# Kernel tuning notes

Hardware: AMD Instinct MI355X
Metric: run time of the kernel (lower is better)

The kernel has to match this reference:

```python
import jax, jax.numpy as jnp
import numpy as np

N = 50000      # nodes
E = 600000     # edges (before self-loops)
D_IN = 128     # input feature dim
HID = 128      # hidden_channels
HEADS1 = 8
OUT1 = HID // HEADS1  # 16 per head, concat -> 128
NEG_SLOPE = 0.2       # PyG GATConv default leaky_relu slope


def setup_inputs() -> dict:
    key = jax.random.key(0)
    ks = jax.random.split(key, 12)
    glorot = lambda k, shape: jax.random.normal(k, shape, jnp.float32) * np.sqrt(2.0 / (shape[0] + shape[-1]))
    x = jax.random.normal(ks[0], (N, D_IN), jnp.float32)
    edge_index = jax.random.randint(ks[1], (2, E), 0, N, dtype=jnp.int64)
    W1 = glorot(ks[2], (D_IN, HEADS1 * OUT1))
    att_src1 = glorot(ks[3], (HEADS1, OUT1))
    att_dst1 = glorot(ks[4], (HEADS1, OUT1))
    b1 = jnp.zeros((HEADS1 * OUT1,), jnp.float32)
    W2 = glorot(ks[5], (HID, HID))
    att_src2 = glorot(ks[6], (1, HID))
    att_dst2 = glorot(ks[7], (1, HID))
    b2 = jnp.zeros((HID,), jnp.float32)
    return {"x": x, "edge_index": edge_index,
            "W1": W1, "att_src1": att_src1, "att_dst1": att_dst1, "b1": b1,
            "W2": W2, "att_src2": att_src2, "att_dst2": att_dst2, "b2": b2}


def gat_conv(x, edge_index, W, a_src, a_dst, bias, concat):
    """PyG-style GATConv (eval mode: attention dropout disabled)."""
    n = x.shape[0]
    heads, out_ch = a_src.shape
    # add self-loops (PyG default add_self_loops=True)
    loop = jnp.arange(n, dtype=edge_index.dtype)
    src = jnp.concatenate([edge_index[0], loop])  # message source
    dst = jnp.concatenate([edge_index[1], loop])  # aggregation target
    h = (x @ W).reshape(n, heads, out_ch)                    # [n, H, C]
    alpha_src = jnp.sum(h * a_src[None], axis=-1)            # [n, H]
    alpha_dst = jnp.sum(h * a_dst[None], axis=-1)            # [n, H]
    e = alpha_src[src] + alpha_dst[dst]                      # [E+n, H]
    e = jnp.where(e > 0, e, NEG_SLOPE * e)                   # leaky_relu
    # segment softmax over incoming edges of each destination node
    e_max = jax.ops.segment_max(e, dst, num_segments=n)      # [n, H]
    ex = jnp.exp(e - e_max[dst])
    denom = jax.ops.segment_sum(ex, dst, num_segments=n)     # [n, H]
    alpha = ex / denom[dst]                                  # [E+n, H]
    msg = h[src] * alpha[:, :, None]                         # [E+n, H, C]
    out = jax.ops.segment_sum(msg, dst, num_segments=n)      # [n, H, C]
    out = out.reshape(n, heads * out_ch) if concat else out.mean(axis=1)
    return out + bias


def reference(x, edge_index, W1, att_src1, att_dst1, b1, W2, att_src2, att_dst2, b2):
    # eval mode: F.dropout is identity
    h = jax.nn.elu(gat_conv(x, edge_index, W1, att_src1, att_dst1, b1, concat=True))
    out = gat_conv(h, edge_index, W2, att_src2, att_dst2, b2, concat=False)
    return out
```

## Files before the change

### kernel.cpp

```cpp
#include <hip/hip_runtime.h>
#include <hip/hip_bf16.h>

#define NEG_SLOPE 0.2f
#define BCAP 8192

typedef short s16x8 __attribute__((ext_vector_type(8)));
typedef float f32x4 __attribute__((ext_vector_type(4)));

__device__ __forceinline__ unsigned short f2bf(float f) {
    unsigned int u = __float_as_uint(f);
    u += 0x7FFFu + ((u >> 16) & 1u);
    return (unsigned short)(u >> 16);
}


__global__ __launch_bounds__(256) void prep_w_kernel(const float* __restrict__ W1,
                                                     const float* __restrict__ as1,
                                                     const float* __restrict__ ad1,
                                                     unsigned short* __restrict__ Wf1,
                                                     const float* __restrict__ W2,
                                                     const float* __restrict__ as2,
                                                     const float* __restrict__ ad2,
                                                     unsigned short* __restrict__ Wf2,
                                                     int* __restrict__ gcursor,
                                                     int* __restrict__ rowptr, int n, int en) {
    int bid = blockIdx.x;
    int t = threadIdx.x;
    if (bid == 8) {
        gcursor[t] = 0;
        if (t == 0) rowptr[n] = en;
        return;
    }
    int layer = bid >> 2;
    int kt = bid & 3;
    const float* W = layer ? W2 : W1;
    const float* as_v = layer ? as2 : as1;
    const float* ad_v = layer ? ad2 : ad1;
    unsigned short* Wf = layer ? Wf2 : Wf1;
    int H = layer ? 1 : 8;
    for (int task = t; task < 9 * 64; task += 256) {
        int ct = task / 64, l = task & 63;
        int kbase = kt * 32 + (l >> 4) * 8;
        int c = l & 15;
        unsigned short o[8];
        if (ct < 8) {
            int col = ct * 16 + c;
#pragma unroll
            for (int j = 0; j < 8; ++j) o[j] = f2bf(W[(size_t)(kbase + j) * 128 + col]);
        } else {
#pragma unroll
            for (int j = 0; j < 8; ++j) {
                float s = 0.f;
                if (H == 8) {
                    const float* a = (c < 8) ? as_v : ad_v;
                    int hh = c & 7;
                    for (int m = 0; m < 16; ++m)
                        s += W[(size_t)(kbase + j) * 128 + hh * 16 + m] * a[hh * 16 + m];
                } else if (c < 2) {
                    const float* a = (c == 0) ? as_v : ad_v;
                    for (int m = 0; m < 128; ++m)
                        s += W[(size_t)(kbase + j) * 128 + m] * a[m];
                }
                o[j] = f2bf(s);
            }
        }
        *(uint4*)&Wf[(((size_t)kt * 9 + ct) * 64 + l) * 8] = *(uint4*)o;
    }
}


__global__ __launch_bounds__(256) void scatter_kernel(const int* __restrict__ ei, int e, int n,
                                                      int* __restrict__ gcursor,
                                                      unsigned int* __restrict__ gpair) {
    __shared__ int lh[256], lbase[256];
    int t = threadIdx.x;
    lh[t] = 0;
    __syncthreads();
    int base = blockIdx.x * 2048;
    int en = e + n;
    int bk[8], rk[8];
    unsigned int pk[8];
#pragma unroll
    for (int q = 0; q < 8; ++q) {
        int i = base + q * 256 + t;
        bk[q] = -1;
        if (i < en) {
            int src, dst;
            if (i < e) { src = ei[i]; dst = ei[e + i]; }
            else       { src = i - e; dst = i - e; }
            int b = dst >> 8;
            bk[q] = b;
            rk[q] = atomicAdd(&lh[b], 1);
            pk[q] = (unsigned int)src | ((unsigned int)(dst & 255) << 16);
        }
    }
    __syncthreads();
    if (lh[t]) lbase[t] = atomicAdd(&gcursor[t], lh[t]);
    __syncthreads();
#pragma unroll
    for (int q = 0; q < 8; ++q)
        if (bk[q] >= 0) gpair[(size_t)bk[q] * BCAP + lbase[bk[q]] + rk[q]] = pk[q];
}


__global__ __launch_bounds__(256) void bucket_csr_kernel(const unsigned int* __restrict__ gpair,
                                                         const int* __restrict__ gcursor,
                                                         int* __restrict__ rowptr,
                                                         int* __restrict__ colsrc, int n) {
    int b = blockIdx.x, t = threadIdx.x;
    __shared__ int bscan[256], cnt[256], scn[256], cur[256];
    int bc = gcursor[t];
    bscan[t] = bc;
    cnt[t] = 0;
    __syncthreads();
    for (int off = 1; off < 256; off <<= 1) {
        int u = (t >= off) ? bscan[t - off] : 0;
        __syncthreads();
        bscan[t] += u;
        __syncthreads();
    }
    int mybase = bscan[b] - gcursor[b];
    int mycnt = gcursor[b];
    const unsigned int* mypair = gpair + (size_t)b * BCAP;
    for (int i = t; i < mycnt; i += 256)
        atomicAdd(&cnt[mypair[i] >> 16], 1);
    __syncthreads();
    int v = cnt[t];
    scn[t] = v;
    __syncthreads();
    for (int off = 1; off < 256; off <<= 1) {
        int u = (t >= off) ? scn[t - off] : 0;
        __syncthreads();
        scn[t] += u;
        __syncthreads();
    }
    int ex = scn[t] - v;
    cur[t] = ex;
    int node = b * 256 + t;
    if (node < n) rowptr[node] = mybase + ex;
    __syncthreads();
    for (int i = t; i < mycnt; i += 256) {
        unsigned int p = mypair[i];
        int ofs = atomicAdd(&cur[p >> 16], 1);
        colsrc[mybase + ofs] = (int)(p & 0xFFFFu);
    }
}


template <int H, bool INBF16>
__global__ __launch_bounds__(256) void gemm_mfma_kernel(const void* __restrict__ Xv,
                                                        const unsigned short* __restrict__ Wf,
                                                        unsigned short* __restrict__ Ob,
                                                        float* __restrict__ as_out,
                                                        float* __restrict__ ad_out, int n) {
    __shared__ unsigned short lds[8192];
    int tid = threadIdx.x;
    int row0 = blockIdx.x * 64;

#pragma unroll
    for (int q = 0; q < 4; ++q) {
        int task = tid + q * 256;
        int r = task >> 4, kc = task & 15;
        int gr = row0 + r;
        uint4 val = make_uint4(0, 0, 0, 0);
        if (gr < n) {
            if (INBF16) {
                val = *(const uint4*)((const unsigned short*)Xv + (size_t)gr * 128 + kc * 8);
            } else {
                const float4* xp = (const float4*)((const float*)Xv + (size_t)gr * 128 + kc * 8);
                float4 x0 = xp[0], x1 = xp[1];
                unsigned short o[8] = {f2bf(x0.x), f2bf(x0.y), f2bf(x0.z), f2bf(x0.w),
                                       f2bf(x1.x), f2bf(x1.y), f2bf(x1.z), f2bf(x1.w)};
                val = *(uint4*)o;
            }
        }
        int w = r >> 4, kt = kc >> 2, lane = ((kc & 3) << 4) + (r & 15);
        *(uint4*)&lds[(size_t)(((w * 4 + kt) * 64) + lane) * 8] = val;
    }
    __syncthreads();

    int w = tid >> 6, l = tid & 63;
    s16x8 a[4];
#pragma unroll
    for (int kt = 0; kt < 4; ++kt)
        a[kt] = *(s16x8*)&lds[(size_t)((w * 4 + kt) * 64 + l) * 8];

    const s16x8* bp = (const s16x8*)Wf;
    f32x4 acc[9];
#pragma unroll
    for (int ct = 0; ct < 9; ++ct) acc[ct] = (f32x4){0.f, 0.f, 0.f, 0.f};
#pragma unroll
    for (int ct = 0; ct < 9; ++ct) {
#pragma unroll
        for (int kt = 0; kt < 4; ++kt) {
            s16x8 b = bp[(kt * 9 + ct) * 64 + l];
            acc[ct] = __builtin_amdgcn_mfma_f32_16x16x32_bf16(a[kt], b, acc[ct], 0, 0, 0);
        }
    }

    int c = l & 15, rgrp = l >> 4;
    int rowb = row0 + w * 16 + rgrp * 4;
#pragma unroll
    for (int reg = 0; reg < 4; ++reg) {
        int row = rowb + reg;
        if (row < n) {
#pragma unroll
            for (int ct = 0; ct < 8; ++ct)
                Ob[(size_t)row * 128 + ct * 16 + c] = f2bf(acc[ct][reg]);
            float av = acc[8][reg];
            if (H == 8) {
                if (c < 8) as_out[(size_t)row * 8 + c] = av;
                else       ad_out[(size_t)row * 8 + (c - 8)] = av;
            } else {
                if (c == 0)      as_out[row] = av;
                else if (c == 1) ad_out[row] = av;
            }
        }
    }
}


template <int H, int OBF>
__global__ __launch_bounds__(256) void agg_kernel(const int* __restrict__ rowptr,
                                                  const int* __restrict__ colsrc,
                                                  const unsigned short* __restrict__ hb,
                                                  const float* __restrict__ as,
                                                  const float* __restrict__ ad,
                                                  const float* __restrict__ bias,
                                                  void* __restrict__ outv, int n) {
    int tid = threadIdx.x;
    int node = blockIdx.x * 16 + (tid >> 4);
    int cl = tid & 15;
    if (node >= n) return;
    int beg = rowptr[node];
    int end = rowptr[node + 1];
    int head = (H == 8) ? (cl >> 1) : 0;
    float adh = ad[(size_t)node * H + head];

    float acc[8];
#pragma unroll
    for (int c = 0; c < 8; ++c) acc[c] = 0.f;
    float den = 0.f;

    int i = beg;
    for (; i + 4 <= end; i += 4) {
        int s0 = colsrc[i], s1 = colsrc[i + 1], s2 = colsrc[i + 2], s3 = colsrc[i + 3];
        float e0 = as[(size_t)s0 * H + head];
        float e1 = as[(size_t)s1 * H + head];
        float e2 = as[(size_t)s2 * H + head];
        float e3 = as[(size_t)s3 * H + head];
        uint4 a0 = *(const uint4*)(hb + (size_t)s0 * 128 + cl * 8);
        uint4 a1 = *(const uint4*)(hb + (size_t)s1 * 128 + cl * 8);
        uint4 a2 = *(const uint4*)(hb + (size_t)s2 * 128 + cl * 8);
        uint4 a3 = *(const uint4*)(hb + (size_t)s3 * 128 + cl * 8);
        float ev, w0, w1, w2, w3;
        ev = e0 + adh; ev = (ev > 0.f) ? ev : NEG_SLOPE * ev; w0 = __expf(ev);
        ev = e1 + adh; ev = (ev > 0.f) ? ev : NEG_SLOPE * ev; w1 = __expf(ev);
        ev = e2 + adh; ev = (ev > 0.f) ? ev : NEG_SLOPE * ev; w2 = __expf(ev);
        ev = e3 + adh; ev = (ev > 0.f) ? ev : NEG_SLOPE * ev; w3 = __expf(ev);
        den += (w0 + w1) + (w2 + w3);
        unsigned int u0[4] = {a0.x, a0.y, a0.z, a0.w};
        unsigned int u1[4] = {a1.x, a1.y, a1.z, a1.w};
        unsigned int u2[4] = {a2.x, a2.y, a2.z, a2.w};
        unsigned int u3[4] = {a3.x, a3.y, a3.z, a3.w};
#pragma unroll
        for (int k = 0; k < 4; ++k) {
            acc[2 * k]     += w0 * __uint_as_float(u0[k] << 16);
            acc[2 * k + 1] += w0 * __uint_as_float(u0[k] & 0xffff0000u);
            acc[2 * k]     += w1 * __uint_as_float(u1[k] << 16);
            acc[2 * k + 1] += w1 * __uint_as_float(u1[k] & 0xffff0000u);
            acc[2 * k]     += w2 * __uint_as_float(u2[k] << 16);
            acc[2 * k + 1] += w2 * __uint_as_float(u2[k] & 0xffff0000u);
            acc[2 * k]     += w3 * __uint_as_float(u3[k] << 16);
            acc[2 * k + 1] += w3 * __uint_as_float(u3[k] & 0xffff0000u);
        }
    }
    for (; i < end; ++i) {
        int s = colsrc[i];
        float ev = as[(size_t)s * H + head] + adh;
        ev = (ev > 0.f) ? ev : NEG_SLOPE * ev;
        float wgt = __expf(ev);
        den += wgt;
        uint4 a = *(const uint4*)(hb + (size_t)s * 128 + cl * 8);
        unsigned int u[4] = {a.x, a.y, a.z, a.w};
#pragma unroll
        for (int k = 0; k < 4; ++k) {
            acc[2 * k]     += wgt * __uint_as_float(u[k] << 16);
            acc[2 * k + 1] += wgt * __uint_as_float(u[k] & 0xffff0000u);
        }
    }

    float inv = 1.0f / den;
    float r[8];
#pragma unroll
    for (int k = 0; k < 8; ++k) {
        r[k] = acc[k] * inv + bias[cl * 8 + k];
        if (OBF) r[k] = (r[k] > 0.f) ? r[k] : expm1f(r[k]);
    }
    if (OBF) {
        unsigned short o[8];
#pragma unroll
        for (int k = 0; k < 8; ++k) o[k] = f2bf(r[k]);
        *(uint4*)((unsigned short*)outv + (size_t)node * 128 + cl * 8) = *(uint4*)o;
    } else {
        float4* p = (float4*)((float*)outv + (size_t)node * 128 + cl * 8);
        p[0] = make_float4(r[0], r[1], r[2], r[3]);
        p[1] = make_float4(r[4], r[5], r[6], r[7]);
    }
}


extern "C" void kernel_launch(void* const* d_in, const int* in_sizes, int n_in,
                              void* d_out, int out_size, void* d_ws, size_t ws_size,
                              hipStream_t stream) {
    const float* x    = (const float*)d_in[0];
    const int*   ei   = (const int*)d_in[1];
    const float* W1   = (const float*)d_in[2];
    const float* a_s1 = (const float*)d_in[3];
    const float* a_d1 = (const float*)d_in[4];
    const float* b1   = (const float*)d_in[5];
    const float* W2   = (const float*)d_in[6];
    const float* a_s2 = (const float*)d_in[7];
    const float* a_d2 = (const float*)d_in[8];
    const float* b2   = (const float*)d_in[9];

    const int n  = in_sizes[0] / 128;
    const int e  = in_sizes[1] / 2;
    const int en = e + n;
    const int nbuck = (n + 255) >> 8;
    const int echunks = (en + 2047) / 2048;

    char* ws = (char*)d_ws;
    size_t off = 0;
    auto alloc = [&](size_t bytes) -> void* {
        void* p = ws + off;
        off += (bytes + 255) & ~(size_t)255;
        return p;
    };
    unsigned short* hb   = (unsigned short*)alloc((size_t)n * 128 * 2);
    unsigned short* hmid = (unsigned short*)alloc((size_t)n * 128 * 2);
    float* as1    = (float*)alloc((size_t)n * 8 * 4);
    float* ad1    = (float*)alloc((size_t)n * 8 * 4);
    float* as2    = (float*)alloc((size_t)n * 4);
    float* ad2    = (float*)alloc((size_t)n * 4);
    int*   rowptr = (int*)alloc((size_t)(n + 1) * 4);
    int*   colsrc = (int*)alloc((size_t)en * 4);
    unsigned int* gpair = (unsigned int*)alloc((size_t)nbuck * BCAP * 4);
    int*   gcursor= (int*)alloc(256 * 4);
    unsigned short* Wf1 = (unsigned short*)alloc(4 * 9 * 64 * 8 * 2);
    unsigned short* Wf2 = (unsigned short*)alloc(4 * 9 * 64 * 8 * 2);

    prep_w_kernel<<<9, 256, 0, stream>>>(W1, a_s1, a_d1, Wf1, W2, a_s2, a_d2, Wf2,
                                         gcursor, rowptr, n, en);
    scatter_kernel<<<echunks, 256, 0, stream>>>(ei, e, n, gcursor, gpair);
    bucket_csr_kernel<<<nbuck, 256, 0, stream>>>(gpair, gcursor, rowptr, colsrc, n);

    int gemm_grid = (n + 63) / 64;
    int node_grid = (n + 15) / 16;

    gemm_mfma_kernel<8, false><<<gemm_grid, 256, 0, stream>>>(x, Wf1, hb, as1, ad1, n);
    agg_kernel<8, 1><<<node_grid, 256, 0, stream>>>(rowptr, colsrc, hb, as1, ad1, b1, hmid, n);

    gemm_mfma_kernel<1, true><<<gemm_grid, 256, 0, stream>>>(hmid, Wf2, hb, as2, ad2, n);
    agg_kernel<1, 0><<<node_grid, 256, 0, stream>>>(rowptr, colsrc, hb, as2, ad2, b2, d_out, n);

    (void)n_in; (void)out_size; (void)ws_size;
}
```

Baseline: 132.0 us.

## Sort nodes by in-degree so aggregation blocks have balanced work

Builds a histogram of node in-degrees during CSR construction, scans it, and writes a degree-sorted node permutation. Both aggregation kernels then process nodes through this order, so the 16 node-groups in a block have similar edge counts and less intra-block imbalance. This adds two small kernels plus an indirection load per node. Output locality is also lost, because consecutive groups now write scattered rows.

```diff
diff --git a/kernel.cpp b/kernel.cpp
--- a/kernel.cpp
+++ b/kernel.cpp
@@ -23,11 +23,13 @@
                                                      const float* __restrict__ ad2,
                                                      unsigned short* __restrict__ Wf2,
                                                      int* __restrict__ gcursor,
+                                                     int* __restrict__ dhist,
                                                      int* __restrict__ rowptr, int n, int en) {
     int bid = blockIdx.x;
     int t = threadIdx.x;
     if (bid == 8) {
         gcursor[t] = 0;
+        dhist[t] = 0;
         if (t == 0) rowptr[n] = en;
         return;
     }
@@ -106,7 +108,8 @@
 __global__ __launch_bounds__(256) void bucket_csr_kernel(const unsigned int* __restrict__ gpair,
                                                          const int* __restrict__ gcursor,
                                                          int* __restrict__ rowptr,
-                                                         int* __restrict__ colsrc, int n) {
+                                                         int* __restrict__ colsrc,
+                                                         int* __restrict__ dhist, int n) {
     int b = blockIdx.x, t = threadIdx.x;
     __shared__ int bscan[256], cnt[256], scn[256], cur[256];
     int bc = gcursor[t];
@@ -137,13 +140,43 @@
     int ex = scn[t] - v;
     cur[t] = ex;
     int node = b * 256 + t;
-    if (node < n) rowptr[node] = mybase + ex;
+    if (node < n) {
+        rowptr[node] = mybase + ex;
+        atomicAdd(&dhist[min(v, 255)], 1);
+    }
     __syncthreads();
     for (int i = t; i < mycnt; i += 256) {
         unsigned int p = mypair[i];
         int ofs = atomicAdd(&cur[p >> 16], 1);
         colsrc[mybase + ofs] = (int)(p & 0xFFFFu);
     }
+}
+
+
+__global__ __launch_bounds__(256) void dscan_kernel(const int* __restrict__ dhist,
+                                                    int* __restrict__ dcursor) {
+    __shared__ int s[256];
+    int t = threadIdx.x;
+    int v = dhist[t];
+    s[t] = v;
+    __syncthreads();
+    for (int off = 1; off < 256; off <<= 1) {
+        int u = (t >= off) ? s[t - off] : 0;
+        __syncthreads();
+        s[t] += u;
+        __syncthreads();
+    }
+    dcursor[t] = s[t] - v;
+}
+
+__global__ __launch_bounds__(256) void dplace_kernel(const int* __restrict__ rowptr,
+                                                     int* __restrict__ dcursor,
+                                                     int* __restrict__ order, int n) {
+    int i = blockIdx.x * blockDim.x + threadIdx.x;
+    if (i >= n) return;
+    int deg = min(rowptr[i + 1] - rowptr[i], 255);
+    int pos = atomicAdd(&dcursor[deg], 1);
+    order[pos] = i;
 }
 
 
@@ -223,15 +256,17 @@
 template <int H, int OBF>
 __global__ __launch_bounds__(256) void agg_kernel(const int* __restrict__ rowptr,
                                                   const int* __restrict__ colsrc,
+                                                  const int* __restrict__ order,
                                                   const unsigned short* __restrict__ hb,
                                                   const float* __restrict__ as,
                                                   const float* __restrict__ ad,
                                                   const float* __restrict__ bias,
                                                   void* __restrict__ outv, int n) {
     int tid = threadIdx.x;
-    int node = blockIdx.x * 16 + (tid >> 4);
+    int idx = blockIdx.x * 16 + (tid >> 4);
     int cl = tid & 15;
-    if (node >= n) return;
+    if (idx >= n) return;
+    int node = order[idx];
     int beg = rowptr[node];
     int end = rowptr[node + 1];
     int head = (H == 8) ? (cl >> 1) : 0;
@@ -347,22 +382,27 @@
     int*   colsrc = (int*)alloc((size_t)en * 4);
     unsigned int* gpair = (unsigned int*)alloc((size_t)nbuck * BCAP * 4);
     int*   gcursor= (int*)alloc(256 * 4);
+    int*   dhist  = (int*)alloc(256 * 4);
+    int*   dcursor= (int*)alloc(256 * 4);
+    int*   order  = (int*)alloc((size_t)n * 4);
     unsigned short* Wf1 = (unsigned short*)alloc(4 * 9 * 64 * 8 * 2);
     unsigned short* Wf2 = (unsigned short*)alloc(4 * 9 * 64 * 8 * 2);
 
     prep_w_kernel<<<9, 256, 0, stream>>>(W1, a_s1, a_d1, Wf1, W2, a_s2, a_d2, Wf2,
-                                         gcursor, rowptr, n, en);
+                                         gcursor, dhist, rowptr, n, en);
     scatter_kernel<<<echunks, 256, 0, stream>>>(ei, e, n, gcursor, gpair);
-    bucket_csr_kernel<<<nbuck, 256, 0, stream>>>(gpair, gcursor, rowptr, colsrc, n);
+    bucket_csr_kernel<<<nbuck, 256, 0, stream>>>(gpair, gcursor, rowptr, colsrc, dhist, n);
+    dscan_kernel<<<1, 256, 0, stream>>>(dhist, dcursor);
+    dplace_kernel<<<(n + 255) / 256, 256, 0, stream>>>(rowptr, dcursor, order, n);
 
     int gemm_grid = (n + 63) / 64;
     int node_grid = (n + 15) / 16;
 
     gemm_mfma_kernel<8, false><<<gemm_grid, 256, 0, stream>>>(x, Wf1, hb, as1, ad1, n);
-    agg_kernel<8, 1><<<node_grid, 256, 0, stream>>>(rowptr, colsrc, hb, as1, ad1, b1, hmid, n);
+    agg_kernel<8, 1><<<node_grid, 256, 0, stream>>>(rowptr, colsrc, order, hb, as1, ad1, b1, hmid, n);
 
     gemm_mfma_kernel<1, true><<<gemm_grid, 256, 0, stream>>>(hmid, Wf2, hb, as2, ad2, n);
-    agg_kernel<1, 0><<<node_grid, 256, 0, stream>>>(rowptr, colsrc, hb, as2, ad2, b2, d_out, n);
+    agg_kernel<1, 0><<<node_grid, 256, 0, stream>>>(rowptr, colsrc, order, hb, as2, ad2, b2, d_out, n);
 
     (void)n_in; (void)out_size; (void)ws_size;
 }
```

New measurement: 443.4 us. +235.9%, slower.
